# Kernel tuning notes

Measured on AMD Instinct MI355X. Metric: run time of the kernel, lower is better.

The kernel has to match this reference:

```python
import jax, jax.numpy as jnp
import numpy as np

B, S, HID = 2, 2048, 4096
NH, NKV, D = 32, 8, 128
G = NH // NKV  # GQA group size = 4
THETA = 10000.0
NEG_INF = -1e30


def _rope(x, positions):
    # Neox-style rotary embedding (vLLM get_rope default). x: [B,S,h,D]
    half = D // 2
    inv_freq = 1.0 / (THETA ** (jnp.arange(half, dtype=jnp.float32) / half))
    freqs = positions[..., None].astype(jnp.float32) * inv_freq  # [B,S,half]
    cos = jnp.cos(freqs)[:, :, None, :]
    sin = jnp.sin(freqs)[:, :, None, :]
    x1, x2 = jnp.split(x, 2, axis=-1)
    return jnp.concatenate([x1 * cos - x2 * sin, x1 * sin + x2 * cos], axis=-1).astype(x.dtype)


def setup_inputs() -> dict:
    key = jax.random.key(0)
    k1, k2, k3 = jax.random.split(key, 3)
    hidden_states = jax.random.normal(k1, (B, S, HID), dtype=jnp.float32)
    w_qkv = jax.random.normal(k2, (HID, NH * D + 2 * NKV * D), dtype=jnp.float32) * 0.02
    w_o = jax.random.normal(k3, (NH * D, HID), dtype=jnp.float32) * 0.02
    positions = jnp.broadcast_to(jnp.arange(S, dtype=jnp.int32), (B, S))
    return {"hidden_states": hidden_states, "w_qkv": w_qkv, "w_o": w_o, "positions": positions}


def reference(hidden_states, w_qkv, w_o, positions):
    qkv = hidden_states @ w_qkv  # [B,S, (NH+2*NKV)*D]
    q = qkv[..., : NH * D].reshape(B, S, NH, D)
    k = qkv[..., NH * D: NH * D + NKV * D].reshape(B, S, NKV, D)
    v = qkv[..., NH * D + NKV * D:].reshape(B, S, NKV, D)
    q = _rope(q, positions)
    k = _rope(k, positions)
    qg = q.reshape(B, S, NKV, G, D)
    scores = jnp.einsum('bqhgd,bkhd->bhgqk', qg, k) * (D ** -0.5)  # [B,NKV,G,S,S]
    causal = jnp.tril(jnp.ones((S, S), dtype=bool))
    scores = jnp.where(causal, scores, NEG_INF)
    attn = jax.nn.softmax(scores, axis=-1)
    out = jnp.einsum('bhgqk,bkhd->bqhgd', attn, v).reshape(B, S, NH * D)
    return out @ w_o  # [B,S,HID]
```

## Files before the change

kernel.cpp:

```cpp
#include <hip/hip_runtime.h>
#include <stdint.h>


#define NB    2
#define SEQ   2048
#define HIDD  4096
#define NHQ   32
#define NKVH  8
#define DHEAD 128
#define NQK   (NHQ * DHEAD)
#define NKVD  (NKVH * DHEAD)
#define NTOT  (NQK + 2 * NKVD)
#define MROWS (NB * SEQ)

typedef unsigned short u16;
typedef _Float16 half8 __attribute__((ext_vector_type(8)));
typedef float f32x4v __attribute__((ext_vector_type(4)));

static __device__ __forceinline__ u16 f2h(float x) {
  _Float16 h = (_Float16)x;
  return __builtin_bit_cast(u16, h);
}

static __device__ __forceinline__ void load_lds16(const void* g, const void* l) {
  __builtin_amdgcn_global_load_lds(
      (const __attribute__((address_space(1))) void*)(uintptr_t)g,
      (__attribute__((address_space(3))) void*)(uintptr_t)l, 16, 0, 0);
}

__global__ __launch_bounds__(256) void k_conv_hs(const float* __restrict__ in,
                                                 u16* __restrict__ out, int n8) {
  int idx = blockIdx.x * 256 + threadIdx.x;
  int stride = gridDim.x * 256;
  for (int i = idx; i < n8; i += stride) {
    const float4* p = (const float4*)(in + (size_t)i * 8);
    float4 a = p[0], b = p[1];
    union { u16 us[8]; int4 v; } t;
    t.us[0] = f2h(a.x); t.us[1] = f2h(a.y); t.us[2] = f2h(a.z); t.us[3] = f2h(a.w);
    t.us[4] = f2h(b.x); t.us[5] = f2h(b.y); t.us[6] = f2h(b.z); t.us[7] = f2h(b.w);
    *(int4*)(out + (size_t)i * 8) = t.v;
  }
}

__global__ __launch_bounds__(256) void k_transpose_f16(const float* __restrict__ in,
                                                       u16* __restrict__ out, int R, int C) {
  __shared__ float tile[64][65];
  int tid = threadIdx.x;
  int c0 = blockIdx.x * 64, r0 = blockIdx.y * 64;
#pragma unroll
  for (int i = 0; i < 4; ++i) {
    int idx = i * 256 + tid;
    int rr = idx >> 4, cc = (idx & 15) * 4;
    float4 v = *(const float4*)&in[(size_t)(r0 + rr) * C + c0 + cc];
    tile[rr][cc] = v.x; tile[rr][cc + 1] = v.y; tile[rr][cc + 2] = v.z; tile[rr][cc + 3] = v.w;
  }
  __syncthreads();
#pragma unroll
  for (int i = 0; i < 4; ++i) {
    int idx = i * 256 + tid;
    int cc = idx >> 4, rr = (idx & 15) * 4;
    union { u16 us[4]; unsigned long long ll; } t;
#pragma unroll
    for (int j = 0; j < 4; ++j) t.us[j] = f2h(tile[rr + j][cc]);
    *(unsigned long long*)&out[(size_t)(c0 + cc) * R + r0 + rr] = t.ll;
  }
}

template <int MODE>
__global__ __launch_bounds__(256, 2) void k_gemm(
    const u16* __restrict__ A, const u16* __restrict__ Bt, int M, int N, int K,
    const int* __restrict__ positions, u16* __restrict__ qout, u16* __restrict__ kout,
    u16* __restrict__ vout, float* __restrict__ Cout) {
  __shared__ u16 As[128 * 64];
  __shared__ u16 Bs[128 * 64];
  const int tid = threadIdx.x;
  const int w = tid >> 6, lane = tid & 63;
  const int lgrp = lane >> 4, l15 = lane & 15;
  const int wr = w >> 1, wc = w & 1;
  const int m0 = blockIdx.y * 128, n0 = blockIdx.x * 128;
  const int srow = lane >> 3, scol = (lane & 7) * 8;
  f32x4v acc[4][4] = {};

  for (int k0 = 0; k0 < K; k0 += 64) {
    __syncthreads();
#pragma unroll
    for (int i = 0; i < 4; ++i) {
      int chunk = w * 4 + i;
      int row = chunk * 8 + srow;
      load_lds16(A + (size_t)(m0 + row) * K + k0 + scol, (const char*)As + chunk * 1024);
      load_lds16(Bt + (size_t)(n0 + row) * K + k0 + scol, (const char*)Bs + chunk * 1024);
    }
    __syncthreads();
#pragma unroll
    for (int kf = 0; kf < 2; ++kf) {
      half8 a[4], b[4];
#pragma unroll
      for (int rf = 0; rf < 4; ++rf)
        a[rf] = *(const half8*)&As[(wr * 64 + rf * 16 + l15) * 64 + kf * 32 + lgrp * 8];
#pragma unroll
      for (int cf = 0; cf < 4; ++cf) {
        int gf = wc * 2 + (cf & 1) + (cf >> 1) * 4;
        b[cf] = *(const half8*)&Bs[(gf * 16 + l15) * 64 + kf * 32 + lgrp * 8];
      }
#pragma unroll
      for (int rf = 0; rf < 4; ++rf)
#pragma unroll
        for (int cf = 0; cf < 4; ++cf)
          acc[rf][cf] = __builtin_amdgcn_mfma_f32_16x16x32_f16(a[rf], b[cf], acc[rf][cf], 0, 0, 0);
    }
  }

  if (MODE == 1) {
#pragma unroll
    for (int rf = 0; rf < 4; ++rf)
#pragma unroll
      for (int cf = 0; cf < 4; ++cf) {
        int gf = wc * 2 + (cf & 1) + (cf >> 1) * 4;
        int col = n0 + gf * 16 + l15;
#pragma unroll
        for (int r = 0; r < 4; ++r) {
          int row = m0 + wr * 64 + rf * 16 + lgrp * 4 + r;
          Cout[(size_t)row * N + col] = acc[rf][cf][r];
        }
      }
  } else {
    const float FREQF = -0.14391156642f;
#pragma unroll
    for (int rf = 0; rf < 4; ++rf) {
#pragma unroll
      for (int r = 0; r < 4; ++r) {
        int row = m0 + wr * 64 + rf * 16 + lgrp * 4 + r;
        int b_ = row >> 11, s = row & (SEQ - 1);
        if (n0 < NQK + NKVD) {
          float pos = (float)positions[row];
#pragma unroll
          for (int cf = 0; cf < 2; ++cf) {
            int gf = wc * 2 + cf;
            int d1 = gf * 16 + l15;
            float ang = pos * expf((float)d1 * FREQF);
            float sn, cs;
            sincosf(ang, &sn, &cs);
            float x1 = acc[rf][cf][r], x2 = acc[rf][cf + 2][r];
            float o1 = x1 * cs - x2 * sn;
            float o2 = x1 * sn + x2 * cs;
            if (n0 < NQK) {
              int h = n0 >> 7;
              size_t base = (((size_t)b_ * NHQ + h) * SEQ + s) * DHEAD;
              qout[base + d1] = f2h(o1);
              qout[base + d1 + 64] = f2h(o2);
            } else {
              int h = (n0 - NQK) >> 7;
              size_t base = (((size_t)b_ * NKVH + h) * SEQ + s) * DHEAD;
              kout[base + d1] = f2h(o1);
              kout[base + d1 + 64] = f2h(o2);
            }
          }
        } else {
          int h = (n0 - NQK - NKVD) >> 7;
          size_t base = ((size_t)b_ * NKVH + h) * DHEAD * SEQ;
#pragma unroll
          for (int cf = 0; cf < 4; ++cf) {
            int gf = wc * 2 + (cf & 1) + (cf >> 1) * 4;
            int d = gf * 16 + l15;
            vout[base + (size_t)d * SEQ + s] = f2h(acc[rf][cf][r]);
          }
        }
      }
    }
  }
}

__global__ __launch_bounds__(256, 2) void k_attn(const u16* __restrict__ Q,
                                                 const u16* __restrict__ Kc,
                                                 const u16* __restrict__ Vct,
                                                 u16* __restrict__ Oout) {
  __shared__ u16 Ks[64 * 136];
  __shared__ u16 Vt[128 * 72];
  __shared__ u16 Pl[64 * 72];
  const int qt = blockIdx.x, h = blockIdx.y, b = blockIdx.z;
  const int hk = h >> 2;
  const int tid = threadIdx.x, w = tid >> 6, lane = tid & 63;
  const int lgrp = lane >> 4, l15 = lane & 15;
  const int q0 = qt * 64;
  const size_t qbase = ((size_t)b * NHQ + h) * SEQ * DHEAD;
  const size_t kbase = ((size_t)b * NKVH + hk) * SEQ * DHEAD;
  const size_t vtbase = ((size_t)b * NKVH + hk) * DHEAD * SEQ;

  half8 qf[4];
  {
    int qrow = q0 + w * 16 + l15;
#pragma unroll
    for (int df = 0; df < 4; ++df)
      qf[df] = *(const half8*)&Q[qbase + (size_t)qrow * DHEAD + df * 32 + lgrp * 8];
  }
  f32x4v O[8] = {};
  float mrow[4], lrow[4];
#pragma unroll
  for (int r = 0; r < 4; ++r) { mrow[r] = -3.0e38f; lrow[r] = 0.f; }

  for (int t = 0; t <= qt; ++t) {
    const int kv0 = t * 64;
    __syncthreads();
#pragma unroll
    for (int i = 0; i < 4; ++i) {
      int idx = i * 256 + tid;
      int kv = idx >> 4, c = idx & 15;
      int4 val = *(const int4*)&Kc[kbase + (size_t)(kv0 + kv) * DHEAD + c * 8];
      *(int4*)&Ks[kv * 136 + c * 8] = val;
    }
#pragma unroll
    for (int i = 0; i < 4; ++i) {
      int idx = i * 256 + tid;
      int d = idx >> 3, c = idx & 7;
      int4 val = *(const int4*)&Vct[vtbase + (size_t)d * SEQ + kv0 + c * 8];
      *(int4*)&Vt[d * 72 + c * 8] = val;
    }
    __syncthreads();

    f32x4v sa[4] = {};
#pragma unroll
    for (int kvf = 0; kvf < 4; ++kvf)
#pragma unroll
      for (int df = 0; df < 4; ++df) {
        half8 kb = *(const half8*)&Ks[(kvf * 16 + l15) * 136 + df * 32 + lgrp * 8];
        sa[kvf] = __builtin_amdgcn_mfma_f32_16x16x32_f16(qf[df], kb, sa[kvf], 0, 0, 0);
      }

    const float scale = 0.08838834764831845f;
#pragma unroll
    for (int r = 0; r < 4; ++r) {
      const int qa = q0 + w * 16 + lgrp * 4 + r;
      float sv[4];
      float mx = -3.0e38f;
#pragma unroll
      for (int kvf = 0; kvf < 4; ++kvf) {
        float x = sa[kvf][r] * scale;
        int ka = kv0 + kvf * 16 + l15;
        x = (ka > qa) ? -3.0e38f : x;
        sv[kvf] = x;
        mx = fmaxf(mx, x);
      }
#pragma unroll
      for (int off = 1; off < 16; off <<= 1) mx = fmaxf(mx, __shfl_xor(mx, off, 64));
      float mnew = fmaxf(mrow[r], mx);
      float alpha = __expf(mrow[r] - mnew);
      mrow[r] = mnew;
      float rs = 0.f;
#pragma unroll
      for (int kvf = 0; kvf < 4; ++kvf) {
        float p = __expf(sv[kvf] - mnew);
        sv[kvf] = p;
        rs += p;
      }
#pragma unroll
      for (int off = 1; off < 16; off <<= 1) rs += __shfl_xor(rs, off, 64);
      lrow[r] = lrow[r] * alpha + rs;
#pragma unroll
      for (int nf = 0; nf < 8; ++nf) O[nf][r] *= alpha;
#pragma unroll
      for (int kvf = 0; kvf < 4; ++kvf)
        Pl[(w * 16 + lgrp * 4 + r) * 72 + kvf * 16 + l15] = f2h(sv[kvf]);
    }

    half8 pa[2];
#pragma unroll
    for (int k2 = 0; k2 < 2; ++k2)
      pa[k2] = *(const half8*)&Pl[(w * 16 + l15) * 72 + k2 * 32 + lgrp * 8];
#pragma unroll
    for (int nf = 0; nf < 8; ++nf)
#pragma unroll
      for (int k2 = 0; k2 < 2; ++k2) {
        half8 vb = *(const half8*)&Vt[(nf * 16 + l15) * 72 + k2 * 32 + lgrp * 8];
        O[nf] = __builtin_amdgcn_mfma_f32_16x16x32_f16(pa[k2], vb, O[nf], 0, 0, 0);
      }
  }

#pragma unroll
  for (int r = 0; r < 4; ++r) {
    float inv = 1.0f / lrow[r];
    int s = q0 + w * 16 + lgrp * 4 + r;
    size_t obase = ((size_t)b * SEQ + s) * NQK + h * DHEAD;
#pragma unroll
    for (int nf = 0; nf < 8; ++nf) Oout[obase + nf * 16 + l15] = f2h(O[nf][r] * inv);
  }
}

extern "C" void kernel_launch(void* const* d_in, const int* in_sizes, int n_in,
                              void* d_out, int out_size, void* d_ws, size_t ws_size,
                              hipStream_t stream) {
  const float* hs = (const float*)d_in[0];
  const float* wqkv = (const float*)d_in[1];
  const float* wo = (const float*)d_in[2];
  const int* positions = (const int*)d_in[3];
  float* out = (float*)d_out;
  char* ws = (char*)d_ws;

  u16* hs16  = (u16*)(ws);
  u16* wqkvt = (u16*)(ws + 33554432);
  u16* q16   = (u16*)(ws + 83886080);
  u16* k16   = (u16*)(ws + 117440512);
  u16* v16t  = (u16*)(ws + 125829120);
  u16* wot    = (u16*)(ws);
  u16* attn16 = (u16*)(ws + 33554432);

  k_conv_hs<<<2048, 256, 0, stream>>>(hs, hs16, MROWS * HIDD / 8);
  k_transpose_f16<<<dim3(NTOT / 64, HIDD / 64), 256, 0, stream>>>(wqkv, wqkvt, HIDD, NTOT);
  k_gemm<0><<<dim3(NTOT / 128, MROWS / 128), 256, 0, stream>>>(
      hs16, wqkvt, MROWS, NTOT, HIDD, positions, q16, k16, v16t, nullptr);
  k_transpose_f16<<<dim3(HIDD / 64, NQK / 64), 256, 0, stream>>>(wo, wot, NQK, HIDD);
  k_attn<<<dim3(SEQ / 64, NHQ, NB), 256, 0, stream>>>(q16, k16, v16t, attn16);
  k_gemm<1><<<dim3(HIDD / 128, MROWS / 128), 256, 0, stream>>>(
      attn16, wot, MROWS, HIDD, NQK, nullptr, nullptr, nullptr, nullptr, out);
}
```

Measured before the change: 1.013 ms.

## Balance causal attention by pairing query tiles per block and reusing LDS

Each attention block now handles two query tiles (qp and 31-qp), so every block does the same amount of causal work. Blocks are launched on a 1D grid with a swizzled block-to-(head,batch,tile) mapping. The P buffer now reuses the K shared-memory region, which lowers LDS use so four blocks can fit per CU, and launch bounds are raised to match. The causal mask is applied only on the diagonal tile, and s_setprio wraps the MFMA sections. In exchange there are extra barriers per iteration, and register pressure may be tighter under the higher occupancy target.

```diff
diff --git a/kernel.cpp b/kernel.cpp
--- a/kernel.cpp
+++ b/kernel.cpp
@@ -170,118 +170,149 @@
   }
 }
 
-__global__ __launch_bounds__(256, 2) void k_attn(const u16* __restrict__ Q,
+__global__ __launch_bounds__(256, 4) void k_attn(const u16* __restrict__ Q,
                                                  const u16* __restrict__ Kc,
                                                  const u16* __restrict__ Vct,
                                                  u16* __restrict__ Oout) {
   __shared__ u16 Ks[64 * 136];
   __shared__ u16 Vt[128 * 72];
-  __shared__ u16 Pl[64 * 72];
-  const int qt = blockIdx.x, h = blockIdx.y, b = blockIdx.z;
-  const int hk = h >> 2;
   const int tid = threadIdx.x, w = tid >> 6, lane = tid & 63;
   const int lgrp = lane >> 4, l15 = lane & 15;
-  const int q0 = qt * 64;
+  const int id = blockIdx.x;
+  const int sw = (id & 7) * 128 + (id >> 3);
+  const int qp = sw & 15, h = (sw >> 4) & 31, b = sw >> 9;
+  const int hk = h >> 2;
   const size_t qbase = ((size_t)b * NHQ + h) * SEQ * DHEAD;
   const size_t kbase = ((size_t)b * NKVH + hk) * SEQ * DHEAD;
   const size_t vtbase = ((size_t)b * NKVH + hk) * DHEAD * SEQ;
-
-  half8 qf[4];
-  {
-    int qrow = q0 + w * 16 + l15;
-#pragma unroll
-    for (int df = 0; df < 4; ++df)
-      qf[df] = *(const half8*)&Q[qbase + (size_t)qrow * DHEAD + df * 32 + lgrp * 8];
-  }
-  f32x4v O[8] = {};
-  float mrow[4], lrow[4];
-#pragma unroll
-  for (int r = 0; r < 4; ++r) { mrow[r] = -3.0e38f; lrow[r] = 0.f; }
-
-  for (int t = 0; t <= qt; ++t) {
-    const int kv0 = t * 64;
-    __syncthreads();
-#pragma unroll
-    for (int i = 0; i < 4; ++i) {
-      int idx = i * 256 + tid;
-      int kv = idx >> 4, c = idx & 15;
-      int4 val = *(const int4*)&Kc[kbase + (size_t)(kv0 + kv) * DHEAD + c * 8];
-      *(int4*)&Ks[kv * 136 + c * 8] = val;
-    }
-#pragma unroll
-    for (int i = 0; i < 4; ++i) {
-      int idx = i * 256 + tid;
-      int d = idx >> 3, c = idx & 7;
-      int4 val = *(const int4*)&Vct[vtbase + (size_t)d * SEQ + kv0 + c * 8];
-      *(int4*)&Vt[d * 72 + c * 8] = val;
-    }
-    __syncthreads();
-
-    f32x4v sa[4] = {};
-#pragma unroll
-    for (int kvf = 0; kvf < 4; ++kvf)
-#pragma unroll
-      for (int df = 0; df < 4; ++df) {
-        half8 kb = *(const half8*)&Ks[(kvf * 16 + l15) * 136 + df * 32 + lgrp * 8];
-        sa[kvf] = __builtin_amdgcn_mfma_f32_16x16x32_f16(qf[df], kb, sa[kvf], 0, 0, 0);
-      }
-
-    const float scale = 0.08838834764831845f;
+  u16* Ps = Ks;
+
+#pragma unroll 1
+  for (int pass = 0; pass < 2; ++pass) {
+    const int qt = pass ? (31 - qp) : qp;
+    const int q0 = qt * 64;
+    half8 qf[4];
+    {
+      int qrow = q0 + w * 16 + l15;
+#pragma unroll
+      for (int df = 0; df < 4; ++df)
+        qf[df] = *(const half8*)&Q[qbase + (size_t)qrow * DHEAD + df * 32 + lgrp * 8];
+    }
+    f32x4v O[8] = {};
+    float mrow[4], lrow[4];
+#pragma unroll
+    for (int r = 0; r < 4; ++r) { mrow[r] = -3.0e38f; lrow[r] = 0.f; }
+
+#pragma unroll 1
+    for (int t = 0; t <= qt; ++t) {
+      const int kv0 = t * 64;
+      __syncthreads();
+#pragma unroll
+      for (int i = 0; i < 4; ++i) {
+        int idx = i * 256 + tid;
+        int kv = idx >> 4, c = idx & 15;
+        int4 val = *(const int4*)&Kc[kbase + (size_t)(kv0 + kv) * DHEAD + c * 8];
+        *(int4*)&Ks[kv * 136 + c * 8] = val;
+      }
+#pragma unroll
+      for (int i = 0; i < 4; ++i) {
+        int idx = i * 256 + tid;
+        int d = idx >> 3, c = idx & 7;
+        int4 val = *(const int4*)&Vct[vtbase + (size_t)d * SEQ + kv0 + c * 8];
+        *(int4*)&Vt[d * 72 + c * 8] = val;
+      }
+      __syncthreads();
+
+      f32x4v sa[4] = {};
+      __builtin_amdgcn_s_setprio(1);
+#pragma unroll
+      for (int kvf = 0; kvf < 4; ++kvf)
+#pragma unroll
+        for (int df = 0; df < 4; ++df) {
+          half8 kb = *(const half8*)&Ks[(kvf * 16 + l15) * 136 + df * 32 + lgrp * 8];
+          sa[kvf] = __builtin_amdgcn_mfma_f32_16x16x32_f16(qf[df], kb, sa[kvf], 0, 0, 0);
+        }
+      __builtin_amdgcn_s_setprio(0);
+
+      const float scale = 0.08838834764831845f;
+      unsigned pv16[4][2];
+#pragma unroll
+      for (int r = 0; r < 4; ++r) {
+        float sv[4];
+        float mx = -3.0e38f;
+        if (t == qt) {
+          const int qa = q0 + w * 16 + lgrp * 4 + r;
+#pragma unroll
+          for (int kvf = 0; kvf < 4; ++kvf) {
+            float x = sa[kvf][r] * scale;
+            int ka = kv0 + kvf * 16 + l15;
+            x = (ka > qa) ? -3.0e38f : x;
+            sv[kvf] = x;
+            mx = fmaxf(mx, x);
+          }
+        } else {
+#pragma unroll
+          for (int kvf = 0; kvf < 4; ++kvf) {
+            float x = sa[kvf][r] * scale;
+            sv[kvf] = x;
+            mx = fmaxf(mx, x);
+          }
+        }
+#pragma unroll
+        for (int off = 1; off < 16; off <<= 1) mx = fmaxf(mx, __shfl_xor(mx, off, 64));
+        float mnew = fmaxf(mrow[r], mx);
+        float alpha = __expf(mrow[r] - mnew);
+        mrow[r] = mnew;
+        float rs = 0.f;
+#pragma unroll
+        for (int kvf = 0; kvf < 4; ++kvf) {
+          float p = __expf(sv[kvf] - mnew);
+          sv[kvf] = p;
+          rs += p;
+        }
+#pragma unroll
+        for (int off = 1; off < 16; off <<= 1) rs += __shfl_xor(rs, off, 64);
+        lrow[r] = lrow[r] * alpha + rs;
+#pragma unroll
+        for (int nf = 0; nf < 8; ++nf) O[nf][r] *= alpha;
+        pv16[r][0] = (unsigned)f2h(sv[0]) | ((unsigned)f2h(sv[1]) << 16);
+        pv16[r][1] = (unsigned)f2h(sv[2]) | ((unsigned)f2h(sv[3]) << 16);
+      }
+
+      __syncthreads();
+#pragma unroll
+      for (int r = 0; r < 4; ++r) {
+        int prow = (w * 16 + lgrp * 4 + r) * 72;
+        Ps[prow + 0 * 16 + l15] = (u16)(pv16[r][0] & 0xffff);
+        Ps[prow + 1 * 16 + l15] = (u16)(pv16[r][0] >> 16);
+        Ps[prow + 2 * 16 + l15] = (u16)(pv16[r][1] & 0xffff);
+        Ps[prow + 3 * 16 + l15] = (u16)(pv16[r][1] >> 16);
+      }
+      __syncthreads();
+
+      half8 pa[2];
+#pragma unroll
+      for (int k2 = 0; k2 < 2; ++k2)
+        pa[k2] = *(const half8*)&Ps[(w * 16 + l15) * 72 + k2 * 32 + lgrp * 8];
+      __builtin_amdgcn_s_setprio(1);
+#pragma unroll
+      for (int nf = 0; nf < 8; ++nf)
+#pragma unroll
+        for (int k2 = 0; k2 < 2; ++k2) {
+          half8 vb = *(const half8*)&Vt[(nf * 16 + l15) * 72 + k2 * 32 + lgrp * 8];
+          O[nf] = __builtin_amdgcn_mfma_f32_16x16x32_f16(pa[k2], vb, O[nf], 0, 0, 0);
+        }
+      __builtin_amdgcn_s_setprio(0);
+    }
+
 #pragma unroll
     for (int r = 0; r < 4; ++r) {
-      const int qa = q0 + w * 16 + lgrp * 4 + r;
-      float sv[4];
-      float mx = -3.0e38f;
-#pragma unroll
-      for (int kvf = 0; kvf < 4; ++kvf) {
-        float x = sa[kvf][r] * scale;
-        int ka = kv0 + kvf * 16 + l15;
-        x = (ka > qa) ? -3.0e38f : x;
-        sv[kvf] = x;
-        mx = fmaxf(mx, x);
-      }
-#pragma unroll
-      for (int off = 1; off < 16; off <<= 1) mx = fmaxf(mx, __shfl_xor(mx, off, 64));
-      float mnew = fmaxf(mrow[r], mx);
-      float alpha = __expf(mrow[r] - mnew);
-      mrow[r] = mnew;
-      float rs = 0.f;
-#pragma unroll
-      for (int kvf = 0; kvf < 4; ++kvf) {
-        float p = __expf(sv[kvf] - mnew);
-        sv[kvf] = p;
-        rs += p;
-      }
-#pragma unroll
-      for (int off = 1; off < 16; off <<= 1) rs += __shfl_xor(rs, off, 64);
-      lrow[r] = lrow[r] * alpha + rs;
-#pragma unroll
-      for (int nf = 0; nf < 8; ++nf) O[nf][r] *= alpha;
-#pragma unroll
-      for (int kvf = 0; kvf < 4; ++kvf)
-        Pl[(w * 16 + lgrp * 4 + r) * 72 + kvf * 16 + l15] = f2h(sv[kvf]);
-    }
-
-    half8 pa[2];
-#pragma unroll
-    for (int k2 = 0; k2 < 2; ++k2)
-      pa[k2] = *(const half8*)&Pl[(w * 16 + l15) * 72 + k2 * 32 + lgrp * 8];
-#pragma unroll
-    for (int nf = 0; nf < 8; ++nf)
-#pragma unroll
-      for (int k2 = 0; k2 < 2; ++k2) {
-        half8 vb = *(const half8*)&Vt[(nf * 16 + l15) * 72 + k2 * 32 + lgrp * 8];
-        O[nf] = __builtin_amdgcn_mfma_f32_16x16x32_f16(pa[k2], vb, O[nf], 0, 0, 0);
-      }
-  }
-
-#pragma unroll
-  for (int r = 0; r < 4; ++r) {
-    float inv = 1.0f / lrow[r];
-    int s = q0 + w * 16 + lgrp * 4 + r;
-    size_t obase = ((size_t)b * SEQ + s) * NQK + h * DHEAD;
-#pragma unroll
-    for (int nf = 0; nf < 8; ++nf) Oout[obase + nf * 16 + l15] = f2h(O[nf][r] * inv);
+      float inv = 1.0f / lrow[r];
+      int s = q0 + w * 16 + lgrp * 4 + r;
+      size_t obase = ((size_t)b * SEQ + s) * NQK + h * DHEAD;
+#pragma unroll
+      for (int nf = 0; nf < 8; ++nf) Oout[obase + nf * 16 + l15] = f2h(O[nf][r] * inv);
+    }
   }
 }
 
@@ -308,7 +339,7 @@
   k_gemm<0><<<dim3(NTOT / 128, MROWS / 128), 256, 0, stream>>>(
       hs16, wqkvt, MROWS, NTOT, HIDD, positions, q16, k16, v16t, nullptr);
   k_transpose_f16<<<dim3(HIDD / 64, NQK / 64), 256, 0, stream>>>(wo, wot, NQK, HIDD);
-  k_attn<<<dim3(SEQ / 64, NHQ, NB), 256, 0, stream>>>(q16, k16, v16t, attn16);
+  k_attn<<<1024, 256, 0, stream>>>(q16, k16, v16t, attn16);
   k_gemm<1><<<dim3(HIDD / 128, MROWS / 128), 256, 0, stream>>>(
       attn16, wot, MROWS, HIDD, NQK, nullptr, nullptr, nullptr, nullptr, out);
 }
```

Result: faster. 881.7 us (-12.9%).
